# Kernel tuning notes

Measured on AMD Instinct MI355X. Metric: run time of the kernel, lower is better.

## Reference

```python
import jax, jax.numpy as jnp
import numpy as np


def setup_inputs() -> dict:
    key = jax.random.key(0)
    k_x, k_q, k_k, k_v = jax.random.split(key, 4)
    B, S, E, D = 4, 2048, 1024, 1024
    scale = 1.0 / np.sqrt(E)
    return {
        "x": jax.random.normal(k_x, (B, S, E), dtype=jnp.float32),
        # nn.Linear weight matrices, shape [out_dim, in_dim]; y = x @ W.T
        "w_q": jax.random.normal(k_q, (D, E), dtype=jnp.float32) * scale,
        "w_k": jax.random.normal(k_k, (D, E), dtype=jnp.float32) * scale,
        "w_v": jax.random.normal(k_v, (D, E), dtype=jnp.float32) * scale,
    }


def reference(x, w_q, w_k, w_v):
    # x: [B, S, E]; w_*: [D, E] (torch nn.Linear convention)
    B, S, E = x.shape
    q = jnp.einsum("bse,de->bsd", x, w_q)  # [B, S, D]
    k = jnp.einsum("bse,de->bsd", x, w_k)
    v = jnp.einsum("bse,de->bsd", x, w_v)
    D = q.shape[-1]
    # raw scores, then causal mask (strictly upper triangle -> -inf), then
    # scale by 1/sqrt(D) inside softmax exactly as the original does.
    scores = jnp.einsum("bsd,btd->bst", q, k)  # [B, S, S]
    causal = jnp.tril(jnp.ones((S, S), dtype=bool))  # True = keep
    scores = jnp.where(causal[None], scores, -jnp.inf)
    attn = jax.nn.softmax(scores / jnp.sqrt(jnp.asarray(D, x.dtype)), axis=-1)
    # dropout p=0.0 -> identity
    return jnp.einsum("bst,btd->bsd", attn, v)  # [B, S, D]
```

## Files before the change

kernel.cpp:

```cpp
#include <hip/hip_runtime.h>
#include <hip/hip_bf16.h>


typedef unsigned short u16;
typedef __attribute__((ext_vector_type(4))) u16   u16x4;
typedef __attribute__((ext_vector_type(8))) u16   u16x8;
typedef __attribute__((ext_vector_type(8))) short short8;
typedef __attribute__((ext_vector_type(4))) float f32x4;
typedef __attribute__((ext_vector_type(4))) int   i32x4;

__device__ inline u16 f2b(float v) {
    __hip_bfloat16 b = __float2bfloat16(v);
    return *reinterpret_cast<u16*>(&b);
}
__device__ inline float b2f(u16 v) {
    unsigned int u = ((unsigned int)v) << 16;
    return *reinterpret_cast<float*>(&u);
}

template <typename T> __device__ inline void store_elem(T* p, float v);
template <> __device__ inline void store_elem<float>(float* p, float v) { *p = v; }
template <> __device__ inline void store_elem<u16>(u16* p, float v)     { *p = f2b(v); }

__device__ inline void gload_lds16(const u16* g, u16* l) {
    __builtin_amdgcn_global_load_lds(
        (const __attribute__((address_space(1))) void*)g,
        (__attribute__((address_space(3))) void*)l, 16, 0, 0);
}

__global__ __launch_bounds__(256) void cast_all_kernel(
    const float* __restrict__ x,  const float* __restrict__ wq,
    const float* __restrict__ wk, const float* __restrict__ wv,
    u16* __restrict__ dst) {
    int q = blockIdx.x * 256 + threadIdx.x;
    const float* src;
    int sidx;
    if (q < 2097152) { src = x; sidx = q * 4; }
    else {
        int qq = q - 2097152;
        int w  = qq >> 18;
        sidx   = (qq & 262143) * 4;
        src    = (w == 0) ? wq : (w == 1) ? wk : wv;
    }
    float4 v = *(const float4*)(src + sidx);
    u16x4 o;
    o.x = f2b(v.x); o.y = f2b(v.y); o.z = f2b(v.z); o.w = f2b(v.w);
    *(u16x4*)(dst + q * 4) = o;
}

#define MT 128
#define NT 128
#define BKH 32
#define HSZ (MT * BKH)

template <typename OutT>
__device__ __forceinline__ void gemm_core(
    const u16* __restrict__ Ab, int lda,
    const u16* __restrict__ Bb, int ldb,
    OutT* __restrict__ Cb, int ldc,
    int m0, int n0, int kbeg, int kend)
{
    __shared__ __align__(16) u16 As[2 * HSZ];
    __shared__ __align__(16) u16 Bs[2 * HSZ];

    const int tid  = threadIdx.x;
    const int lane = tid & 63;
    const int wave = tid >> 6;
    const int quad = lane >> 4;
    const int r16  = lane & 15;
    const int mw   = (wave >> 1) * 64;
    const int nw   = (wave & 1) * 64;

    const int c0 = tid, c1 = tid + 256;
    const int r0 = c0 >> 2, k0 = (c0 & 3) * 8;
    const int r1 = c1 >> 2, k1 = (c1 & 3) * 8;
    const int oa0 = (m0 + r0) * lda + k0;
    const int oa1 = (m0 + r1) * lda + k1;
    const int ob0 = (n0 + r0) * ldb + k0;
    const int ob1 = (n0 + r1) * ldb + k1;

    f32x4 acc[4][4] = {};

    for (int kk = kbeg; kk < kend; kk += 2 * BKH) {
        __syncthreads();
        gload_lds16(Ab + (kk + oa0),        &As[c0 * 8]);
        gload_lds16(Ab + (kk + oa1),        &As[c1 * 8]);
        gload_lds16(Ab + (kk + BKH + oa0),  &As[HSZ + c0 * 8]);
        gload_lds16(Ab + (kk + BKH + oa1),  &As[HSZ + c1 * 8]);
        gload_lds16(Bb + (kk + ob0),        &Bs[c0 * 8]);
        gload_lds16(Bb + (kk + ob1),        &Bs[c1 * 8]);
        gload_lds16(Bb + (kk + BKH + ob0),  &Bs[HSZ + c0 * 8]);
        gload_lds16(Bb + (kk + BKH + ob1),  &Bs[HSZ + c1 * 8]);
        __syncthreads();

#pragma unroll
        for (int h = 0; h < 2; h++) {
            short8 af[4], bf[4];
#pragma unroll
            for (int i = 0; i < 4; i++)
                af[i] = *(const short8*)&As[h * HSZ + (mw + i * 16 + r16) * BKH + quad * 8];
#pragma unroll
            for (int j = 0; j < 4; j++)
                bf[j] = *(const short8*)&Bs[h * HSZ + (nw + j * 16 + r16) * BKH + quad * 8];
#pragma unroll
            for (int i = 0; i < 4; i++)
#pragma unroll
                for (int j = 0; j < 4; j++)
                    acc[i][j] = __builtin_amdgcn_mfma_f32_16x16x32_bf16(af[i], bf[j], acc[i][j], 0, 0, 0);
        }
    }

#pragma unroll
    for (int i = 0; i < 4; i++)
#pragma unroll
        for (int j = 0; j < 4; j++)
#pragma unroll
            for (int r = 0; r < 4; r++) {
                int m = m0 + mw + i * 16 + quad * 4 + r;
                int n = n0 + nw + j * 16 + r16;
                store_elem(&Cb[(long long)m * ldc + n], acc[i][j][r]);
            }
}

__global__ __launch_bounds__(256, 4) void gemm_qkv(
    const u16* __restrict__ A, const u16* __restrict__ B, u16* __restrict__ C) {
    gemm_core<u16>(A, 1024, B, 1024, C, 3072,
                   blockIdx.y * MT, blockIdx.x * NT, 0, 1024);
}

__global__ __launch_bounds__(256, 4) void gemm_scores(
    const u16* __restrict__ qkv, u16* __restrict__ sc) {
    int t = blockIdx.x;
    float ff = sqrtf(8.0f * t + 1.0f);
    int m = (int)((ff - 1.0f) * 0.5f);
    while ((m + 1) * (m + 2) / 2 <= t) m++;
    while (m * (m + 1) / 2 > t) m--;
    int m0 = m * MT;
    int n0 = (t - m * (m + 1) / 2) * NT;
    const u16* Ab = qkv + (long long)blockIdx.z * 2048 * 3072;
    const u16* Bb = Ab + 1024;
    u16* Cb = sc + (long long)blockIdx.z * 2048 * 2048;
    gemm_core<u16>(Ab, 3072, Bb, 3072, Cb, 2048, m0, n0, 0, 1024);
}

__global__ __launch_bounds__(256, 4) void gemm_pv(
    const u16* __restrict__ P, const u16* __restrict__ vt,
    float* __restrict__ out, float* __restrict__ part)
{
    const int bid = blockIdx.x;
    int m, chunk, n;
    if (bid < 80) {
        int q = bid >> 3; n = bid & 7;
        if (q < 9) { m = 7 + q; chunk = 0; } else { m = 15; chunk = 1; }
    } else {
        int r = bid - 80; int s = 7 - (r >> 4); int t = r & 15;
        n = t & 7;
        if (t < 8) { m = s - 1; chunk = 0; } else { m = s + 7; chunk = 1; }
    }
    const int m0 = m * MT, n0 = n * NT;
    const int kbeg = chunk ? 1024 : 0;
    const int kend = chunk ? (m0 + MT) : min(1024, m0 + MT);
    const int b = blockIdx.z;

    const u16* Ab = P  + (long long)b * 2048 * 2048;
    const u16* Bb = vt + (long long)b * 1024 * 2048;
    if (chunk == 0) {
        float* Cb = out + (long long)b * 2097152;
        gemm_core<float>(Ab, 2048, Bb, 2048, Cb, 1024, m0, n0, kbeg, kend);
    } else {
        float* Cb = part + (long long)b * 1048576 - 1024LL * 1024;
        gemm_core<float>(Ab, 2048, Bb, 2048, Cb, 1024, m0, n0, kbeg, kend);
    }
}

__global__ __launch_bounds__(256) void pv_combine(float* __restrict__ out,
                                                  const float* __restrict__ part) {
    long long idx = ((long long)blockIdx.x * 256 + threadIdx.x) * 8;
    long long bb = idx >> 20;
    long long j  = idx & 1048575;
    float* o = out + bb * 2097152 + 1048576 + j;
    const float* p = part + bb * 1048576 + j;
    float4 o0 = *(float4*)o, o1 = *(float4*)(o + 4);
    float4 p0 = *(const float4*)p, p1 = *(const float4*)(p + 4);
    o0.x += p0.x; o0.y += p0.y; o0.z += p0.z; o0.w += p0.w;
    o1.x += p1.x; o1.y += p1.y; o1.z += p1.z; o1.w += p1.w;
    *(float4*)o = o0; *(float4*)(o + 4) = o1;
}

__global__ __launch_bounds__(256) void softmax_kernel(const u16* __restrict__ sc,
                                                      u16* __restrict__ P) {
    const int S = 2048;
    int row = blockIdx.x;
    int i   = row & (S - 1);
    int n   = i + 1;
    const u16* srow = sc + (long long)row * S;
    u16*       prow = P  + (long long)row * S;

    int j0 = threadIdx.x * 8;
    u16x8 raw = *(const u16x8*)(srow + j0);
    float v[8];
#pragma unroll
    for (int e = 0; e < 8; e++) v[e] = (j0 + e < n) ? b2f(raw[e]) : -1e30f;

    __shared__ float red[8];
    float lmax = v[0];
#pragma unroll
    for (int e = 1; e < 8; e++) lmax = fmaxf(lmax, v[e]);
    for (int o = 32; o > 0; o >>= 1) lmax = fmaxf(lmax, __shfl_xor(lmax, o, 64));
    int wid = threadIdx.x >> 6;
    if ((threadIdx.x & 63) == 0) red[wid] = lmax;
    __syncthreads();
    float Mx = fmaxf(fmaxf(red[0], red[1]), fmaxf(red[2], red[3]));

    const float C = 0.045112384f;
    float ev[8];
    float lsum = 0.f;
#pragma unroll
    for (int e = 0; e < 8; e++) {
        ev[e] = (j0 + e < n) ? exp2f((v[e] - Mx) * C) : 0.f;
        lsum += ev[e];
    }
    for (int o = 32; o > 0; o >>= 1) lsum += __shfl_xor(lsum, o, 64);
    if ((threadIdx.x & 63) == 0) red[4 + wid] = lsum;
    __syncthreads();
    float inv = 1.0f / (red[4] + red[5] + red[6] + red[7]);

    u16x8 o8;
#pragma unroll
    for (int e = 0; e < 8; e++) o8[e] = f2b(ev[e] * inv);
    *(u16x8*)(prow + j0) = o8;
}

__global__ __launch_bounds__(256) void transpose_v_kernel(const u16* __restrict__ qkv,
                                                          u16* __restrict__ vt) {
    int b  = blockIdx.z;
    int s0 = blockIdx.x * 64;
    int d0 = blockIdx.y * 64;
    __shared__ __align__(16) u16 tile[64][80];
    int tid = threadIdx.x;
    for (int c = tid; c < 512; c += 256) {
        int r = c >> 3, c8 = (c & 7) * 8;
        *(i32x4*)&tile[r][c8] =
            *(const i32x4*)(qkv + (long long)(b * 2048 + s0 + r) * 3072 + 2048 + d0 + c8);
    }
    __syncthreads();
    for (int c = tid; c < 512; c += 256) {
        int dd = c >> 3, s8 = (c & 7) * 8;
        alignas(16) u16 tmp[8];
#pragma unroll
        for (int e = 0; e < 8; e++) tmp[e] = tile[s8 + e][dd];
        *(i32x4*)(vt + ((long long)b * 1024 + d0 + dd) * 2048 + s0 + s8) = *(i32x4*)tmp;
    }
}

extern "C" void kernel_launch(void* const* d_in, const int* in_sizes, int n_in,
                              void* d_out, int out_size, void* d_ws, size_t ws_size,
                              hipStream_t stream) {
    const float* x  = (const float*)d_in[0];
    const float* wq = (const float*)d_in[1];
    const float* wk = (const float*)d_in[2];
    const float* wv = (const float*)d_in[3];
    float* out = (float*)d_out;

    char* ws = (char*)d_ws;
    u16*   xb   = (u16*)(ws);
    u16*   wb   = (u16*)(ws + 16777216LL);
    u16*   qkv  = (u16*)(ws + 23068672LL);
    u16*   sc   = (u16*)(ws + 73400320LL);
    u16*   P    = (u16*)(ws + 106954752LL);
    u16*   vt   = (u16*)(ws + 140509184LL);
    float* part = (float*)(ws + 157286400LL);

    cast_all_kernel<<<11264, 256, 0, stream>>>(x, wq, wk, wv, xb);

    gemm_qkv<<<dim3(24, 64, 1), 256, 0, stream>>>(xb, wb, qkv);

    transpose_v_kernel<<<dim3(32, 16, 4), 256, 0, stream>>>(qkv, vt);

    gemm_scores<<<dim3(136, 1, 4), 256, 0, stream>>>(qkv, sc);

    softmax_kernel<<<8192, 256, 0, stream>>>(sc, P);

    gemm_pv<<<dim3(192, 1, 4), 256, 0, stream>>>(P, vt, out, part);
    pv_combine<<<2048, 256, 0, stream>>>(out, part);
}
```

Measured before the change: 263.3 us.

## Write V transposed from QKV GEMM epilogue and skip masked softmax traffic

The QKV projection GEMM now writes Q and K into a compact [B*S, 2048] buffer and writes V directly in transposed [B, D, S] layout from its epilogue, so the separate transpose kernel and its extra read/write of V are removed. The softmax kernel now loads only the causal part of each score row and writes probabilities only up to the end of the row's 128-column tile, which is all the PV GEMM reads. The cost is that the transposed epilogue stores 4-element strided vectors, which coalesce less well than row-major stores.

Measured after the change: 255.9 us. 1.03x faster.

```diff
diff --git a/kernel.cpp b/kernel.cpp
--- a/kernel.cpp
+++ b/kernel.cpp
@@ -53,7 +53,7 @@
 #define BKH 32
 #define HSZ (MT * BKH)
 
-template <typename OutT>
+template <int TRANS, typename OutT>
 __device__ __forceinline__ void gemm_core(
     const u16* __restrict__ Ab, int lda,
     const u16* __restrict__ Bb, int ldb,
@@ -110,26 +110,47 @@
         }
     }
 
-#pragma unroll
-    for (int i = 0; i < 4; i++)
-#pragma unroll
-        for (int j = 0; j < 4; j++)
-#pragma unroll
-            for (int r = 0; r < 4; r++) {
-                int m = m0 + mw + i * 16 + quad * 4 + r;
-                int n = n0 + nw + j * 16 + r16;
-                store_elem(&Cb[(long long)m * ldc + n], acc[i][j][r]);
+    if (TRANS == 0) {
+#pragma unroll
+        for (int i = 0; i < 4; i++)
+#pragma unroll
+            for (int j = 0; j < 4; j++)
+#pragma unroll
+                for (int r = 0; r < 4; r++) {
+                    int m = m0 + mw + i * 16 + quad * 4 + r;
+                    int n = n0 + nw + j * 16 + r16;
+                    store_elem(&Cb[(long long)m * ldc + n], acc[i][j][r]);
+                }
+    } else {
+#pragma unroll
+        for (int i = 0; i < 4; i++)
+#pragma unroll
+            for (int j = 0; j < 4; j++) {
+                int mbase = m0 + mw + i * 16 + quad * 4;
+                int d     = n0 + nw + j * 16 + r16;
+                int b     = mbase >> 11;
+                int s     = mbase & 2047;
+                u16x4 o;
+#pragma unroll
+                for (int r = 0; r < 4; r++) o[r] = f2b(acc[i][j][r]);
+                *(u16x4*)((u16*)Cb + (((b << 10) + d) * 2048 + s)) = o;
             }
+    }
 }
 
 __global__ __launch_bounds__(256, 4) void gemm_qkv(
-    const u16* __restrict__ A, const u16* __restrict__ B, u16* __restrict__ C) {
-    gemm_core<u16>(A, 1024, B, 1024, C, 3072,
-                   blockIdx.y * MT, blockIdx.x * NT, 0, 1024);
+    const u16* __restrict__ xb, const u16* __restrict__ wb,
+    u16* __restrict__ qk, u16* __restrict__ vt) {
+    int bx = blockIdx.x, m0 = blockIdx.y * MT;
+    if (bx < 16)
+        gemm_core<0, u16>(xb, 1024, wb, 1024, qk, 2048, m0, bx * 128, 0, 1024);
+    else
+        gemm_core<1, u16>(xb, 1024, wb + 2048 * 1024, 1024, vt, 2048,
+                          m0, (bx - 16) * 128, 0, 1024);
 }
 
 __global__ __launch_bounds__(256, 4) void gemm_scores(
-    const u16* __restrict__ qkv, u16* __restrict__ sc) {
+    const u16* __restrict__ qk, u16* __restrict__ sc) {
     int t = blockIdx.x;
     float ff = sqrtf(8.0f * t + 1.0f);
     int m = (int)((ff - 1.0f) * 0.5f);
@@ -137,10 +158,10 @@
     while (m * (m + 1) / 2 > t) m--;
     int m0 = m * MT;
     int n0 = (t - m * (m + 1) / 2) * NT;
-    const u16* Ab = qkv + (long long)blockIdx.z * 2048 * 3072;
+    const u16* Ab = qk + (long long)blockIdx.z * 2048 * 2048;
     const u16* Bb = Ab + 1024;
     u16* Cb = sc + (long long)blockIdx.z * 2048 * 2048;
-    gemm_core<u16>(Ab, 3072, Bb, 3072, Cb, 2048, m0, n0, 0, 1024);
+    gemm_core<0, u16>(Ab, 2048, Bb, 2048, Cb, 2048, m0, n0, 0, 1024);
 }
 
 __global__ __launch_bounds__(256, 4) void gemm_pv(
@@ -166,10 +187,10 @@
     const u16* Bb = vt + (long long)b * 1024 * 2048;
     if (chunk == 0) {
         float* Cb = out + (long long)b * 2097152;
-        gemm_core<float>(Ab, 2048, Bb, 2048, Cb, 1024, m0, n0, kbeg, kend);
+        gemm_core<0, float>(Ab, 2048, Bb, 2048, Cb, 1024, m0, n0, kbeg, kend);
     } else {
         float* Cb = part + (long long)b * 1048576 - 1024LL * 1024;
-        gemm_core<float>(Ab, 2048, Bb, 2048, Cb, 1024, m0, n0, kbeg, kend);
+        gemm_core<0, float>(Ab, 2048, Bb, 2048, Cb, 1024, m0, n0, kbeg, kend);
     }
 }
 
@@ -193,11 +214,13 @@
     int row = blockIdx.x;
     int i   = row & (S - 1);
     int n   = i + 1;
+    int kendr = (i & ~127) + 128;
     const u16* srow = sc + (long long)row * S;
     u16*       prow = P  + (long long)row * S;
 
     int j0 = threadIdx.x * 8;
-    u16x8 raw = *(const u16x8*)(srow + j0);
+    u16x8 raw = {};
+    if (j0 <= i) raw = *(const u16x8*)(srow + j0);
     float v[8];
 #pragma unroll
     for (int e = 0; e < 8; e++) v[e] = (j0 + e < n) ? b2f(raw[e]) : -1e30f;
@@ -225,31 +248,11 @@
     __syncthreads();
     float inv = 1.0f / (red[4] + red[5] + red[6] + red[7]);
 
-    u16x8 o8;
-#pragma unroll
-    for (int e = 0; e < 8; e++) o8[e] = f2b(ev[e] * inv);
-    *(u16x8*)(prow + j0) = o8;
-}
-
-__global__ __launch_bounds__(256) void transpose_v_kernel(const u16* __restrict__ qkv,
-                                                          u16* __restrict__ vt) {
-    int b  = blockIdx.z;
-    int s0 = blockIdx.x * 64;
-    int d0 = blockIdx.y * 64;
-    __shared__ __align__(16) u16 tile[64][80];
-    int tid = threadIdx.x;
-    for (int c = tid; c < 512; c += 256) {
-        int r = c >> 3, c8 = (c & 7) * 8;
-        *(i32x4*)&tile[r][c8] =
-            *(const i32x4*)(qkv + (long long)(b * 2048 + s0 + r) * 3072 + 2048 + d0 + c8);
-    }
-    __syncthreads();
-    for (int c = tid; c < 512; c += 256) {
-        int dd = c >> 3, s8 = (c & 7) * 8;
-        alignas(16) u16 tmp[8];
-#pragma unroll
-        for (int e = 0; e < 8; e++) tmp[e] = tile[s8 + e][dd];
-        *(i32x4*)(vt + ((long long)b * 1024 + d0 + dd) * 2048 + s0 + s8) = *(i32x4*)tmp;
+    if (j0 < kendr) {
+        u16x8 o8;
+#pragma unroll
+        for (int e = 0; e < 8; e++) o8[e] = f2b(ev[e] * inv);
+        *(u16x8*)(prow + j0) = o8;
     }
 }
 
@@ -265,19 +268,17 @@
     char* ws = (char*)d_ws;
     u16*   xb   = (u16*)(ws);
     u16*   wb   = (u16*)(ws + 16777216LL);
-    u16*   qkv  = (u16*)(ws + 23068672LL);
-    u16*   sc   = (u16*)(ws + 73400320LL);
-    u16*   P    = (u16*)(ws + 106954752LL);
-    u16*   vt   = (u16*)(ws + 140509184LL);
-    float* part = (float*)(ws + 157286400LL);
+    u16*   qk   = (u16*)(ws + 23068672LL);
+    u16*   sc   = (u16*)(ws + 56623104LL);
+    u16*   P    = (u16*)(ws + 90177536LL);
+    u16*   vt   = (u16*)(ws + 123731968LL);
+    float* part = (float*)(ws + 140509184LL);
 
     cast_all_kernel<<<11264, 256, 0, stream>>>(x, wq, wk, wv, xb);
 
-    gemm_qkv<<<dim3(24, 64, 1), 256, 0, stream>>>(xb, wb, qkv);
-
-    transpose_v_kernel<<<dim3(32, 16, 4), 256, 0, stream>>>(qkv, vt);
-
-    gemm_scores<<<dim3(136, 1, 4), 256, 0, stream>>>(qkv, sc);
+    gemm_qkv<<<dim3(24, 64, 1), 256, 0, stream>>>(xb, wb, qk, vt);
+
+    gemm_scores<<<dim3(136, 1, 4), 256, 0, stream>>>(qk, sc);
 
     softmax_kernel<<<8192, 256, 0, stream>>>(sc, P);
 
```
